# Performance work log

Measured on AMD Instinct MI355X. Metric: run time of the kernel, lower is better.

Reference implementation:

```python
import jax, jax.numpy as jnp
import numpy as np

B, N, D_IN, D, H = 4, 256, 600, 600, 256  # batch, nodes, in_dim, mem_dim, attn hidden


def setup_inputs() -> dict:
    key = jax.random.key(0)
    ks = jax.random.split(key, 12)
    feature = jax.random.normal(ks[0], (B, N, D_IN), dtype=jnp.float32)
    latent_adj = jax.random.randint(ks[1], (B, N, N), 0, 2).astype(jnp.float32)
    s_in = 1.0 / np.sqrt(D_IN)
    s_d = 1.0 / np.sqrt(D)
    s_2d = 1.0 / np.sqrt(2 * D)
    s_h = 1.0 / np.sqrt(H)
    W0 = jax.random.uniform(ks[2], (D_IN, D), jnp.float32, -s_in, s_in)
    b0 = jax.random.uniform(ks[3], (D,), jnp.float32, -s_in, s_in)
    W1 = jax.random.uniform(ks[4], (D, D), jnp.float32, -s_d, s_d)
    b1 = jax.random.uniform(ks[5], (D,), jnp.float32, -s_d, s_d)
    aW1 = jax.random.uniform(ks[6], (2 * D, H), jnp.float32, -s_2d, s_2d)
    ab1 = jax.random.uniform(ks[7], (H,), jnp.float32, -s_2d, s_2d)
    aW2 = jax.random.uniform(ks[8], (H,), jnp.float32, -s_h, s_h)
    ab2 = jax.random.uniform(ks[9], (1,), jnp.float32, -s_h, s_h)
    return {"feature": feature, "latent_adj": latent_adj, "W0": W0, "b0": b0,
            "W1": W1, "b1": b1, "aW1": aW1, "ab1": ab1, "aW2": aW2, "ab2": ab2}


def _gat_layer(x, Wl, bl, aW1, ab1, aW2, ab2, adj):
    h = jnp.einsum('bni,io->bno', x, Wl) + bl                    # [B,N,D]
    # Decompose first attn linear: [h_i, h_j] @ aW1 = h_i @ aW1[:D] + h_j @ aW1[D:]
    left = jnp.einsum('bnd,dh->bnh', h, aW1[:h.shape[-1]])        # i-part
    right = jnp.einsum('bnd,dh->bnh', h, aW1[h.shape[-1]:])       # j-part
    hid = jax.nn.relu(left[:, :, None, :] + right[:, None, :, :] + ab1)  # [B,N,N,H]
    e = jax.nn.leaky_relu(jnp.einsum('bijh,h->bij', hid, aW2) + ab2[0],
                          negative_slope=0.01)                    # [B,N,N]
    e = jnp.where(adj == 0, jnp.float32(-1e9), e)
    attention = jax.nn.softmax(e, axis=-1) * adj
    return jax.nn.relu(jnp.einsum('bij,bjd->bid', attention, h))


def reference(feature, latent_adj, W0, b0, W1, b1, aW1, ab1, aW2, ab2):
    h = _gat_layer(feature, W0, b0, aW1, ab1, aW2, ab2, latent_adj)
    h = _gat_layer(h, W1, b1, aW1, ab1, aW2, ab2, latent_adj)
    return h
```

## Files before the change

kernel.cpp:

```cpp
#include <hip/hip_runtime.h>
#include <hip/hip_bf16.h>

#define BATCH 4
#define NN    256
#define DD    600
#define HH    256
#define MROWS (BATCH*NN)
#define KPAD  640
#define ATTS  272

typedef __attribute__((ext_vector_type(8))) short bf16x8;
typedef __attribute__((ext_vector_type(4))) float f32x4;

__device__ __forceinline__ void gload16(const void* g, void* l)
{
    __builtin_amdgcn_global_load_lds(
        (const __attribute__((address_space(1))) void*)g,
        (__attribute__((address_space(3))) void*)l, 16, 0, 0);
}

__device__ __forceinline__ void waitcnt_vm(int n)
{
    switch (n) {
    case 0:  asm volatile("s_waitcnt vmcnt(0)"  ::: "memory"); break;
    case 3:  asm volatile("s_waitcnt vmcnt(3)"  ::: "memory"); break;
    case 4:  asm volatile("s_waitcnt vmcnt(4)"  ::: "memory"); break;
    case 6:  asm volatile("s_waitcnt vmcnt(6)"  ::: "memory"); break;
    default: asm volatile("s_waitcnt vmcnt(0)"  ::: "memory"); break;
    }
}

__device__ __forceinline__ int xcd_remap(int lin, int nwg)
{
    const int q = nwg >> 3, r = nwg & 7;
    const int xcd = lin & 7, off = lin >> 3;
    return (xcd < r ? xcd * (q + 1) : r * (q + 1) + (xcd - r) * q) + off;
}

template<bool BIAS, bool WF32, bool WB16, bool WHT, int NK>
__global__ __launch_bounds__(256) void gemm_mfma(
    const __hip_bfloat16* __restrict__ A, const __hip_bfloat16* __restrict__ BT,
    const float* __restrict__ bias,
    float* __restrict__ Cf, __hip_bfloat16* __restrict__ Cb,
    __hip_bfloat16* __restrict__ hT,
    int lda, int ldb, int ldcf, int ldcb, int Nvalid, int biasN)
{
    __shared__ __align__(16) char lds[49152];

    const int nwg = gridDim.x * gridDim.y;
    int lin = xcd_remap(blockIdx.x + gridDim.x * blockIdx.y, nwg);
    const int bx = lin % gridDim.x;
    const int by = lin / gridDim.x;

    const int tid  = threadIdx.x;
    const int lane = tid & 63;
    const int wid  = tid >> 6;
    const int wr   = wid >> 1;
    const int wc   = wid & 1;
    const int row0 = by * 64;
    const int col0 = bx * 32;

    const char* Ab = (const char*)A + ((long long)row0 * lda) * 2;
    const char* Bb = (const char*)BT + ((long long)col0 * ldb) * 2;

    const int sr   = tid >> 3;
    const int scb  = (tid & 7) * 16;
    const int scbs = scb ^ ((sr & 7) << 4);

    const char* gA0 = Ab + (long long)sr        * (lda * 2) + scbs;
    const char* gA1 = Ab + (long long)(sr + 32) * (lda * 2) + scbs;
    const char* gB0 = Bb + (long long)sr        * (ldb * 2) + scbs;

    f32x4 acc[2] = {};
    const int fr = lane & 15;
    const int kg = (lane >> 4) * 16;
    const int xv = (fr & 7) << 4;

    auto issue = [&](int t) {
        char* bA = lds + (t & 3) * 8192;
        char* bB = lds + 32768 + (t & 3) * 4096;
        const long long off = (long long)t * 128;
        gload16(gA0 + off, bA + wid * 1024);
        gload16(gA1 + off, bA + 4096 + wid * 1024);
        gload16(gB0 + off, bB + wid * 1024);
    };

    constexpr int PRE = (NK < 3) ? NK : 3;
    #pragma unroll
    for (int p = 0; p < PRE; ++p) issue(p);

    #pragma unroll
    for (int t = 0; t < NK; ++t) {
        const int imax = (t + 2 < NK - 1) ? t + 2 : NK - 1;
        waitcnt_vm(3 * (imax - t));
        __builtin_amdgcn_s_barrier();
        const char* lA = lds + (t & 3) * 8192;
        const char* lB = lds + 32768 + (t & 3) * 4096;
        #pragma unroll
        for (int ks = 0; ks < 2; ++ks) {
            const int kb = ks * 64 + kg;
            bf16x8 a0 = *(const bf16x8*)(lA + (wr * 32 + fr)      * 128 + (kb ^ xv));
            bf16x8 a1 = *(const bf16x8*)(lA + (wr * 32 + 16 + fr) * 128 + (kb ^ xv));
            bf16x8 b0 = *(const bf16x8*)(lB + (wc * 16 + fr)      * 128 + (kb ^ xv));
            acc[0] = __builtin_amdgcn_mfma_f32_16x16x32_bf16(a0, b0, acc[0], 0, 0, 0);
            acc[1] = __builtin_amdgcn_mfma_f32_16x16x32_bf16(a1, b0, acc[1], 0, 0, 0);
        }
        if (t + 3 < NK) issue(t + 3);
    }
    __syncthreads();

    const int er = (lane >> 4) * 4;
    const int ec = lane & 15;
    __hip_bfloat16* sT = (__hip_bfloat16*)lds;

    #pragma unroll
    for (int mi = 0; mi < 2; ++mi) {
        const int lr0 = wr * 32 + mi * 16 + er;
        const int lc  = wc * 16 + ec;
        const int gr = row0 + lr0;
        const int gc = col0 + lc;
        const float bv = (BIAS && gc < biasN) ? bias[gc] : 0.f;
        #pragma unroll
        for (int r = 0; r < 4; ++r) {
            float v = acc[mi][r] + bv;
            const __hip_bfloat16 hv = __float2bfloat16(v);
            const long long row = gr + r;
            if (WF32 && gc < Nvalid)
                Cf[row * ldcf + gc] = v;
            if (WB16)
                Cb[row * ldcb + gc] = hv;
            if (WHT)
                sT[(lr0 + r) * 40 + lc] = hv;
        }
    }

    if (WHT) {
        __syncthreads();
        const int b  = row0 >> 8;
        const int i0 = row0 & 255;
        const int cc = tid >> 3;
        const int ch = tid & 7;
        const int d = col0 + cc;
        __align__(16) __hip_bfloat16 tmp[8];
        #pragma unroll
        for (int u = 0; u < 8; ++u)
            tmp[u] = sT[(ch * 8 + u) * 40 + cc];
        *(float4*)&hT[((long long)b * KPAD + d) * NN + i0 + ch * 8] = *(float4*)tmp;
    }
}

__global__ __launch_bounds__(256) void prep_kernel(
    const float* __restrict__ feature, const float* __restrict__ W0,
    const float* __restrict__ W1, const float* __restrict__ aW1,
    __hip_bfloat16* __restrict__ xb, __hip_bfloat16* __restrict__ W0T,
    __hip_bfloat16* __restrict__ W1T, __hip_bfloat16* __restrict__ aW1T)
{
    const int bid = blockIdx.x;
    const int tid = threadIdx.x;
    if (bid < 640) {
        const int idx = (bid * 256 + tid) * 4;
        const int r = idx / KPAD, c = idx % KPAD;
        float4 v = make_float4(0.f, 0.f, 0.f, 0.f);
        if (c < DD) v = *(const float4*)&feature[r * DD + c];
        __align__(8) __hip_bfloat16 o[4] = {
            __float2bfloat16(v.x), __float2bfloat16(v.y),
            __float2bfloat16(v.z), __float2bfloat16(v.w)};
        *(float2*)&xb[idx] = *(float2*)o;
        return;
    }
    __shared__ float tile[32][33];
    const int t = bid - 640;
    const int which = (t < 400) ? 0 : (t < 800) ? 1 : 2;
    const int tt = (which == 0) ? t : (which == 1) ? t - 400 : t - 800;
    const int n0 = (tt / 20) * 32;
    const int k0 = (tt % 20) * 32;
    const int tx = tid & 31, ty = tid >> 5;
    #pragma unroll
    for (int r = 0; r < 4; ++r) {
        const int k = k0 + ty + r * 8;
        const int n = n0 + tx;
        float v = 0.f;
        if (which == 0)      { if (k < DD && n < DD) v = W0[k * DD + n]; }
        else if (which == 1) { if (k < DD && n < DD) v = W1[k * DD + n]; }
        else                 { if (k < DD) v = (n < HH) ? aW1[k * HH + n]
                                                        : aW1[(DD + k) * HH + (n - HH)]; }
        tile[ty + r * 8][tx] = v;
    }
    __syncthreads();
    __hip_bfloat16* dst = (which == 0) ? W0T : (which == 1) ? W1T : aW1T;
    #pragma unroll
    for (int r = 0; r < 4; ++r) {
        const int n = n0 + ty + r * 8;
        const int k = k0 + tx;
        dst[n * KPAD + k] = __float2bfloat16(tile[tx][ty + r * 8]);
    }
}

__device__ __forceinline__ void block_max4(float* v, float (*red)[4])
{
    #pragma unroll
    for (int o = 32; o > 0; o >>= 1)
        #pragma unroll
        for (int q = 0; q < 4; ++q) v[q] = fmaxf(v[q], __shfl_down(v[q], o));
    const int lane = threadIdx.x & 63, w = threadIdx.x >> 6;
    if (lane == 0) { red[w][0]=v[0]; red[w][1]=v[1]; red[w][2]=v[2]; red[w][3]=v[3]; }
    __syncthreads();
    #pragma unroll
    for (int q = 0; q < 4; ++q)
        v[q] = fmaxf(fmaxf(red[0][q], red[1][q]), fmaxf(red[2][q], red[3][q]));
    __syncthreads();
}

__device__ __forceinline__ void block_sum4(float* v, float (*red)[4])
{
    #pragma unroll
    for (int o = 32; o > 0; o >>= 1)
        #pragma unroll
        for (int q = 0; q < 4; ++q) v[q] += __shfl_down(v[q], o);
    const int lane = threadIdx.x & 63, w = threadIdx.x >> 6;
    if (lane == 0) { red[w][0]=v[0]; red[w][1]=v[1]; red[w][2]=v[2]; red[w][3]=v[3]; }
    __syncthreads();
    #pragma unroll
    for (int q = 0; q < 4; ++q)
        v[q] = red[0][q] + red[1][q] + red[2][q] + red[3][q];
    __syncthreads();
}

template<bool OUTF32>
__global__ __launch_bounds__(256) void attn_pv(
    const float* __restrict__ LR, const float* __restrict__ aW2,
    const float* __restrict__ ab2, const float* __restrict__ adj,
    const __hip_bfloat16* __restrict__ hT,
    __hip_bfloat16* __restrict__ Ob, float* __restrict__ Of)
{
    __shared__ __align__(16) char smem[57344];
    float (*sL)[HH] = (float(*)[HH])(smem + 49152);
    float* sW       = (float*)(smem + 49152 + 4096);
    float (*red)[4] = (float(*)[4])(smem + 49152 + 5120);
    __hip_bfloat16* attl = (__hip_bfloat16*)(smem + 49152 + 5120 + 64);

    const int b  = blockIdx.y;
    const int i0 = blockIdx.x * 4;
    const int j  = threadIdx.x;
    const int tid  = threadIdx.x;
    const int lane = tid & 63;
    const int wid  = tid >> 6;

    float a[4];
    #pragma unroll
    for (int q = 0; q < 4; ++q)
        a[q] = adj[((long long)(b * NN + i0 + q)) * NN + j];
    const float ab2v = ab2[0];

    sW[j] = aW2[j];
    #pragma unroll
    for (int q = 0; q < 4; ++q)
        sL[q][j] = LR[((long long)(b * NN + i0 + q)) * 512 + j];
    __syncthreads();

    const float* rp = LR + ((long long)(b * NN + j)) * 512 + HH;
    float acs[4] = {0.f, 0.f, 0.f, 0.f};
    for (int h = 0; h < HH; h += 8) {
        const float4 ra = *(const float4*)(rp + h);
        const float4 rb = *(const float4*)(rp + h + 4);
        const float4 w0 = *(const float4*)&sW[h];
        const float4 w1 = *(const float4*)&sW[h + 4];
        #pragma unroll
        for (int q = 0; q < 4; ++q) {
            const float4 l0 = *(const float4*)&sL[q][h];
            const float4 l1 = *(const float4*)&sL[q][h + 4];
            float s = fmaxf(l0.x + ra.x, 0.f) * w0.x;
            s += fmaxf(l0.y + ra.y, 0.f) * w0.y;
            s += fmaxf(l0.z + ra.z, 0.f) * w0.z;
            s += fmaxf(l0.w + ra.w, 0.f) * w0.w;
            s += fmaxf(l1.x + rb.x, 0.f) * w1.x;
            s += fmaxf(l1.y + rb.y, 0.f) * w1.y;
            s += fmaxf(l1.z + rb.z, 0.f) * w1.z;
            s += fmaxf(l1.w + rb.w, 0.f) * w1.w;
            acs[q] += s;
        }
    }

    float m[4];
    #pragma unroll
    for (int q = 0; q < 4; ++q) {
        float e = acs[q] + ab2v;
        e = (e > 0.f) ? e : 0.01f * e;
        m[q] = (a[q] == 0.f) ? -1e9f : e;
    }
    float mx[4] = {m[0], m[1], m[2], m[3]};
    block_max4(mx, red);
    float p[4];
    #pragma unroll
    for (int q = 0; q < 4; ++q) p[q] = __expf(m[q] - mx[q]);
    float s4[4] = {p[0], p[1], p[2], p[3]};
    block_sum4(s4, red);

    #pragma unroll
    for (int q = 0; q < 4; ++q)
        attl[q * ATTS + j] = __float2bfloat16(p[q] / s4[q] * a[q]);

    asm volatile("s_waitcnt lgkmcnt(0)" ::: "memory");
    asm volatile("s_waitcnt vmcnt(0)" ::: "memory");
    __builtin_amdgcn_s_barrier();

    const char* hTb = (const char*)(hT + (long long)b * KPAD * NN);
    const int rsub = wid * 4 + (lane >> 4);
    const int cb16 = (lane & 15) * 16;

    auto stage = [&](int c) {
        char* buf = smem + (c % 3) * 16384;
        const int d0 = (c >> 1) * 64;
        const int ko = (c & 1) * 256;
        #pragma unroll
        for (int i = 0; i < 4; ++i) {
            const int r = i * 16 + rsub;
            gload16(hTb + (long long)(d0 + r) * 512 + ko + (cb16 ^ ((r & 7) << 4)),
                    buf + i * 4096 + wid * 1024);
        }
    };

    f32x4 acc[10] = {};
    const int fr = lane & 15;
    const int kg = (lane >> 4) * 16;
    const int xv = (fr & 7) << 4;
    const int arow = lane & 15;

    stage(0); stage(1);
    #pragma unroll
    for (int c = 0; c < 20; ++c) {
        waitcnt_vm(c < 19 ? 4 : 0);
        __builtin_amdgcn_s_barrier();
        const char* buf = smem + (c % 3) * 16384;
        const int t  = c >> 1;
        const int kt = c & 1;
        #pragma unroll
        for (int ks = 0; ks < 4; ++ks) {
            const int kb = ks * 64 + kg;
            bf16x8 bfr = *(const bf16x8*)(buf + (wid * 16 + fr) * 256 + (kb ^ xv));
            bf16x8 afr = {};
            if (arow < 4)
                afr = *(const bf16x8*)((const char*)attl + arow * (ATTS * 2)
                                       + (kt * 128 + ks * 32 + (lane >> 4) * 8) * 2);
            acc[t] = __builtin_amdgcn_mfma_f32_16x16x32_bf16(afr, bfr, acc[t], 0, 0, 0);
        }
        if (c + 2 < 20) stage(c + 2);
    }

    if ((lane >> 4) == 0) {
        #pragma unroll
        for (int t = 0; t < 10; ++t) {
            const int gc = t * 64 + wid * 16 + (lane & 15);
            #pragma unroll
            for (int r = 0; r < 4; ++r) {
                const float v = fmaxf(acc[t][r], 0.f);
                const long long row = (long long)(b * NN + i0 + r);
                if (OUTF32) {
                    if (gc < DD) Of[row * DD + gc] = v;
                } else {
                    Ob[row * KPAD + gc] = __float2bfloat16(v);
                }
            }
        }
    }
}

extern "C" void kernel_launch(void* const* d_in, const int* in_sizes, int n_in,
                              void* d_out, int out_size, void* d_ws, size_t ws_size,
                              hipStream_t stream)
{
    const float* feature = (const float*)d_in[0];
    const float* adj     = (const float*)d_in[1];
    const float* W0      = (const float*)d_in[2];
    const float* b0      = (const float*)d_in[3];
    const float* W1      = (const float*)d_in[4];
    const float* b1      = (const float*)d_in[5];
    const float* aW1     = (const float*)d_in[6];
    const float* ab1     = (const float*)d_in[7];
    const float* aW2     = (const float*)d_in[8];
    const float* ab2     = (const float*)d_in[9];
    float* out = (float*)d_out;

    __hip_bfloat16* bw = (__hip_bfloat16*)d_ws;
    __hip_bfloat16* xb   = bw;
    __hip_bfloat16* W0T  = xb   + MROWS * KPAD;
    __hip_bfloat16* W1T  = W0T  + KPAD * KPAD;
    __hip_bfloat16* aW1T = W1T  + KPAD * KPAD;
    __hip_bfloat16* hb   = aW1T + 512 * KPAD;
    __hip_bfloat16* hT   = hb   + MROWS * KPAD;
    float* LR = (float*)(hT + BATCH * KPAD * NN);

    prep_kernel<<<1760, 256, 0, stream>>>(feature, W0, W1, aW1, xb, W0T, W1T, aW1T);

    for (int layer = 0; layer < 2; ++layer) {
        const __hip_bfloat16* WT = layer ? W1T : W0T;
        const float* bb          = layer ? b1 : b0;

        gemm_mfma<true, false, true, true, KPAD/64>
            <<<dim3(KPAD / 32, MROWS / 64), 256, 0, stream>>>(
            xb, WT, bb, nullptr, hb, hT,
            KPAD, KPAD, 0, KPAD, 0, DD);

        gemm_mfma<true, true, false, false, KPAD/64>
            <<<dim3(512 / 32, MROWS / 64), 256, 0, stream>>>(
            hb, aW1T, ab1, LR, nullptr, nullptr,
            KPAD, KPAD, 512, 0, 512, HH);

        if (layer == 0) {
            attn_pv<false><<<dim3(NN / 4, BATCH), 256, 0, stream>>>(
                LR, aW2, ab2, adj, hT, xb, nullptr);
        } else {
            attn_pv<true><<<dim3(NN / 4, BATCH), 256, 0, stream>>>(
                LR, aW2, ab2, adj, hT, nullptr, out);
        }
    }
}
```

Before: 74.42 us.

## Load hT fragments directly from global in attn_pv, dropping LDS staging

The PV stage of the attention kernel no longer stages hT tiles through a triple-buffered LDS pipeline with global_load_lds and barriers. Each wave now owns a contiguous 160-column slice of D and reads B fragments straight from global memory, with the attention row fragment hoisted per k-step. This removes the 48KB LDS buffer and the per-step barriers, which may improve occupancy. The cost is uncoalesced global loads with less latency hiding, and the loss of the swizzled staging layout.

```diff
diff --git a/kernel.cpp b/kernel.cpp
--- a/kernel.cpp
+++ b/kernel.cpp
@@ -24,7 +24,6 @@
     switch (n) {
     case 0:  asm volatile("s_waitcnt vmcnt(0)"  ::: "memory"); break;
     case 3:  asm volatile("s_waitcnt vmcnt(3)"  ::: "memory"); break;
-    case 4:  asm volatile("s_waitcnt vmcnt(4)"  ::: "memory"); break;
     case 6:  asm volatile("s_waitcnt vmcnt(6)"  ::: "memory"); break;
     default: asm volatile("s_waitcnt vmcnt(0)"  ::: "memory"); break;
     }
@@ -233,18 +232,16 @@
     const __hip_bfloat16* __restrict__ hT,
     __hip_bfloat16* __restrict__ Ob, float* __restrict__ Of)
 {
-    __shared__ __align__(16) char smem[57344];
-    float (*sL)[HH] = (float(*)[HH])(smem + 49152);
-    float* sW       = (float*)(smem + 49152 + 4096);
-    float (*red)[4] = (float(*)[4])(smem + 49152 + 5120);
-    __hip_bfloat16* attl = (__hip_bfloat16*)(smem + 49152 + 5120 + 64);
+    __shared__ float sL[4][HH];
+    __shared__ float sW[HH];
+    __shared__ float red[4][4];
+    __shared__ __align__(16) __hip_bfloat16 attl[4 * ATTS];
 
     const int b  = blockIdx.y;
     const int i0 = blockIdx.x * 4;
     const int j  = threadIdx.x;
-    const int tid  = threadIdx.x;
-    const int lane = tid & 63;
-    const int wid  = tid >> 6;
+    const int lane = threadIdx.x & 63;
+    const int wid  = threadIdx.x >> 6;
 
     float a[4];
     #pragma unroll
@@ -299,61 +296,34 @@
     #pragma unroll
     for (int q = 0; q < 4; ++q)
         attl[q * ATTS + j] = __float2bfloat16(p[q] / s4[q] * a[q]);
-
-    asm volatile("s_waitcnt lgkmcnt(0)" ::: "memory");
-    asm volatile("s_waitcnt vmcnt(0)" ::: "memory");
-    __builtin_amdgcn_s_barrier();
+    __syncthreads();
 
     const char* hTb = (const char*)(hT + (long long)b * KPAD * NN);
-    const int rsub = wid * 4 + (lane >> 4);
-    const int cb16 = (lane & 15) * 16;
-
-    auto stage = [&](int c) {
-        char* buf = smem + (c % 3) * 16384;
-        const int d0 = (c >> 1) * 64;
-        const int ko = (c & 1) * 256;
-        #pragma unroll
-        for (int i = 0; i < 4; ++i) {
-            const int r = i * 16 + rsub;
-            gload16(hTb + (long long)(d0 + r) * 512 + ko + (cb16 ^ ((r & 7) << 4)),
-                    buf + i * 4096 + wid * 1024);
-        }
-    };
+    const int fr  = lane & 15;
+    const int kgb = (lane >> 4) * 16;
+    const int ar  = (fr < 4) ? fr : 0;
+    const char* pa = (const char*)attl + ar * (ATTS * 2) + kgb;
+    const int d0w = wid * 160;
 
     f32x4 acc[10] = {};
-    const int fr = lane & 15;
-    const int kg = (lane >> 4) * 16;
-    const int xv = (fr & 7) << 4;
-    const int arow = lane & 15;
-
-    stage(0); stage(1);
-    #pragma unroll
-    for (int c = 0; c < 20; ++c) {
-        waitcnt_vm(c < 19 ? 4 : 0);
-        __builtin_amdgcn_s_barrier();
-        const char* buf = smem + (c % 3) * 16384;
-        const int t  = c >> 1;
-        const int kt = c & 1;
-        #pragma unroll
-        for (int ks = 0; ks < 4; ++ks) {
-            const int kb = ks * 64 + kg;
-            bf16x8 bfr = *(const bf16x8*)(buf + (wid * 16 + fr) * 256 + (kb ^ xv));
-            bf16x8 afr = {};
-            if (arow < 4)
-                afr = *(const bf16x8*)((const char*)attl + arow * (ATTS * 2)
-                                       + (kt * 128 + ks * 32 + (lane >> 4) * 8) * 2);
-            acc[t] = __builtin_amdgcn_mfma_f32_16x16x32_bf16(afr, bfr, acc[t], 0, 0, 0);
-        }
-        if (c + 2 < 20) stage(c + 2);
+    #pragma unroll
+    for (int kt = 0; kt < 8; ++kt) {
+        const bf16x8 afr = *(const bf16x8*)(pa + kt * 64);
+        #pragma unroll
+        for (int nt = 0; nt < 10; ++nt) {
+            const int d = d0w + nt * 16 + fr;
+            const bf16x8 bfr = *(const bf16x8*)(hTb + (long long)d * 512 + kt * 64 + kgb);
+            acc[nt] = __builtin_amdgcn_mfma_f32_16x16x32_bf16(afr, bfr, acc[nt], 0, 0, 0);
+        }
     }
 
     if ((lane >> 4) == 0) {
         #pragma unroll
-        for (int t = 0; t < 10; ++t) {
-            const int gc = t * 64 + wid * 16 + (lane & 15);
+        for (int nt = 0; nt < 10; ++nt) {
+            const int gc = d0w + nt * 16 + fr;
             #pragma unroll
             for (int r = 0; r < 4; ++r) {
-                const float v = fmaxf(acc[t][r], 0.f);
+                const float v = fmaxf(acc[nt][r], 0.f);
                 const long long row = (long long)(b * NN + i0 + r);
                 if (OUTF32) {
                     if (gc < DD) Of[row * DD + gc] = v;
```

Result: slower. 79.07 us (+6.2%).
